# Kernel optimization log

Hardware: AMD Instinct MI355X
Metric: run time of the kernel (lower is better)

Reference implementation:

```python
import jax, jax.numpy as jnp
import numpy as np

B, TRG, SRC, ENC, TRGD = 16, 512, 1024, 1024, 1024


def setup_inputs() -> dict:
    key = jax.random.key(0)
    k1, k2, k3, k4, k5 = jax.random.split(key, 5)
    hidden = jax.random.normal(k1, (B, TRG, TRGD), dtype=jnp.float32)
    encoder_outputs = jax.random.normal(k2, (B, SRC, ENC), dtype=jnp.float32)
    encoder_value = jax.random.normal(k3, (B, SRC, TRGD), dtype=jnp.float32)
    # float {0,1} padding mask over source positions; keep first token valid
    encoder_mask = (jax.random.uniform(k4, (B, SRC)) > 0.15).astype(jnp.float32)
    encoder_mask = encoder_mask.at[:, :1].set(1.0)
    # nn.Linear(enc_dim, trg_dim, bias=False).weight -> (trg_dim, enc_dim)
    W = jax.random.normal(k5, (TRGD, ENC), dtype=jnp.float32) * (1.0 / np.sqrt(ENC))
    return {"hidden": hidden, "encoder_outputs": encoder_outputs,
            "encoder_value": encoder_value, "encoder_mask": encoder_mask, "W": W}


def reference(hidden, encoder_outputs, encoder_value, encoder_mask, W):
    # score(): method == 'general'
    proj = jnp.einsum('bse,te->bst', encoder_outputs, W)          # (B, S, trg_dim)
    proj = proj * encoder_mask[:, :, None]                        # mask-multiply projected keys
    energies = jnp.einsum('btd,bsd->bts', hidden, proj)           # (B, T, S)
    # forward(): second mask-multiply on raw energies
    attn_energies = energies * encoder_mask[:, None, :]
    # masked_softmax(x, m, -1): x*m -> stable exp -> *m -> normalize (+eps)
    x = attn_energies * encoder_mask[:, None, :]
    e = jnp.exp(x - jnp.max(x, axis=-1, keepdims=True))
    e = e * encoder_mask[:, None, :]
    attn_weights = e / (jnp.sum(e, axis=-1, keepdims=True) + 1e-6)
    context = jnp.einsum('bts,bsd->btd', attn_weights, encoder_value)  # (B, T, trg_dim)
    return context, attn_weights, attn_energies
```

## Files before the change

kernel.cpp:

```cpp
#include <hip/hip_runtime.h>
#include <math.h>

#define B_  16
#define T_  512
#define S_  1024
#define E_  1024
#define D_  1024

using short8   = __attribute__((ext_vector_type(8))) short;
using ushort4v = __attribute__((ext_vector_type(4))) unsigned short;
using float4v  = __attribute__((ext_vector_type(4))) float;

__device__ __forceinline__ unsigned short f2bf(float f) {
    unsigned u = __builtin_bit_cast(unsigned, f);
    u += 0x7fff + ((u >> 16) & 1);
    return (unsigned short)(u >> 16);
}

__device__ __forceinline__ void gl_lds16(const void* g, void* l) {
    __builtin_amdgcn_global_load_lds(
        (const __attribute__((address_space(1))) void*)g,
        (__attribute__((address_space(3))) void*)l, 16, 0, 0);
}

__global__ __launch_bounds__(256)
void cast_bf16(const float* __restrict__ src, unsigned short* __restrict__ dst, int n8)
{
    int i = blockIdx.x * 256 + threadIdx.x;
    if (i < n8) {
        float4 a = ((const float4*)src)[2 * i];
        float4 b = ((const float4*)src)[2 * i + 1];
        short8 o;
        o[0] = f2bf(a.x); o[1] = f2bf(a.y); o[2] = f2bf(a.z); o[3] = f2bf(a.w);
        o[4] = f2bf(b.x); o[5] = f2bf(b.y); o[6] = f2bf(b.z); o[7] = f2bf(b.w);
        ((short8*)dst)[i] = o;
    }
}

__global__ __launch_bounds__(256)
void transpose_cast(const float* __restrict__ src, unsigned short* __restrict__ dst,
                    int R, int C, long long sSrc, long long sDst)
{
    __shared__ unsigned short tile[64][65];
    const int z = blockIdx.z;
    src += (long long)z * sSrc;
    dst += (long long)z * sDst;
    const int c0 = blockIdx.x * 64;
    const int r0 = blockIdx.y * 64;
    const int t = threadIdx.x;

    #pragma unroll
    for (int it = 0; it < 4; ++it) {
        int r  = (t >> 4) + it * 16;
        int c4 = (t & 15) << 2;
        float4 v = *(const float4*)&src[(long long)(r0 + r) * C + c0 + c4];
        tile[r][c4 + 0] = f2bf(v.x);
        tile[r][c4 + 1] = f2bf(v.y);
        tile[r][c4 + 2] = f2bf(v.z);
        tile[r][c4 + 3] = f2bf(v.w);
    }
    __syncthreads();
    #pragma unroll
    for (int it = 0; it < 2; ++it) {
        int c  = (t >> 3) + it * 32;
        int r8 = (t & 7) << 3;
        short8 sv;
        #pragma unroll
        for (int j = 0; j < 8; ++j) sv[j] = (short)tile[r8 + j][c];
        *(short8*)&dst[(long long)(c0 + c) * R + r0 + r8] = sv;
    }
}

template<bool OUT_BF16, bool CMASK>
__global__ __launch_bounds__(256, 2)
void mfma_gemm_bf(const unsigned short* __restrict__ Ap,
                  const unsigned short* __restrict__ Bp,
                  const float* __restrict__ mask, void* __restrict__ Cp,
                  int N, int K,
                  long long sA, long long sB, long long sC, int maskStride)
{
    __shared__ unsigned short Asl[2][2 * 128 * 32];
    __shared__ unsigned short Bsl[2][2 * 128 * 32];

    const int z    = blockIdx.z;
    const int col0 = blockIdx.x * 128;
    const int row0 = blockIdx.y * 128;
    const int t    = threadIdx.x;
    const int lane = t & 63;
    const int wave = t >> 6;

    const unsigned short* A  = Ap + z * sA + (long long)row0 * K;
    const unsigned short* Bm = Bp + z * sB + (long long)col0 * K;

    const int rs  = t >> 2;
    const int kcs = (t & 3) << 3;
    const unsigned ldsW = wave * 1024;

    const int wm = (wave >> 1) * 64;
    const int wn = (wave & 1) * 64;
    const int fr = lane & 15;
    const int fg = lane >> 4;

    float4v acc[4][4];
    #pragma unroll
    for (int i = 0; i < 4; ++i)
        #pragma unroll
        for (int j = 0; j < 4; ++j)
            acc[i][j] = (float4v)0.0f;

    auto STAGE = [&](int bufi, int k0) {
        #pragma unroll
        for (int j = 0; j < 2; ++j) {
            #pragma unroll
            for (int it = 0; it < 2; ++it) {
                const int r = rs + it * 64;
                const long long goff = (long long)r * K + k0 + j * 32 + kcs;
                const unsigned loff = j * 8192 + it * 4096 + ldsW;
                gl_lds16(A  + goff, (char*)&Asl[bufi][0] + loff);
                gl_lds16(Bm + goff, (char*)&Bsl[bufi][0] + loff);
            }
        }
    };

    auto COMPUTE = [&](int bufi) {
        short8 af[2][4], bfr[2][4];
        #pragma unroll
        for (int j = 0; j < 2; ++j) {
            #pragma unroll
            for (int mi = 0; mi < 4; ++mi)
                af[j][mi] = *(const short8*)&Asl[bufi][j * 4096 + (wm + mi * 16 + fr) * 32 + fg * 8];
            #pragma unroll
            for (int ni = 0; ni < 4; ++ni)
                bfr[j][ni] = *(const short8*)&Bsl[bufi][j * 4096 + (wn + ni * 16 + fr) * 32 + fg * 8];
        }
        #pragma unroll
        for (int j = 0; j < 2; ++j)
            #pragma unroll
            for (int mi = 0; mi < 4; ++mi)
                #pragma unroll
                for (int ni = 0; ni < 4; ++ni)
                    acc[mi][ni] = __builtin_amdgcn_mfma_f32_16x16x32_bf16(af[j][mi], bfr[j][ni], acc[mi][ni], 0, 0, 0);
    };

    STAGE(0, 0);
    __syncthreads();

    int buf = 0;
    for (int k0 = 64; k0 <= K; k0 += 64) {
        if (k0 < K) STAGE(buf ^ 1, k0);
        COMPUTE(buf);
        __syncthreads();
        buf ^= 1;
    }

    float mv[4];
    #pragma unroll
    for (int ni = 0; ni < 4; ++ni) {
        int ocol = col0 + wn + ni * 16 + fr;
        mv[ni] = CMASK ? mask[(long long)z * maskStride + ocol] : 1.0f;
    }
    #pragma unroll
    for (int mi = 0; mi < 4; ++mi) {
        #pragma unroll
        for (int ni = 0; ni < 4; ++ni) {
            int ocol = col0 + wn + ni * 16 + fr;
            #pragma unroll
            for (int r = 0; r < 4; ++r) {
                int orow = row0 + wm + mi * 16 + fg * 4 + r;
                float v = acc[mi][ni][r] * mv[ni];
                if (OUT_BF16)
                    ((unsigned short*)Cp)[z * sC + (long long)orow * N + ocol] = f2bf(v);
                else
                    ((float*)Cp)[z * sC + (long long)orow * N + ocol] = v;
            }
        }
    }
}

__global__ __launch_bounds__(256)
void softmax_mask(const float* __restrict__ x, const float* __restrict__ mask,
                  float* __restrict__ w, unsigned short* __restrict__ wbf)
{
    const int row = blockIdx.x;
    const int b   = row >> 9;
    const float* xr = x    + (long long)row * S_;
    const float* mr = mask + (long long)b * S_;
    float*       wr = w    + (long long)row * S_;
    const int tid = threadIdx.x;

    float4 xv = ((const float4*)xr)[tid];
    float4 mv = ((const float4*)mr)[tid];

    float lmax = fmaxf(fmaxf(xv.x, xv.y), fmaxf(xv.z, xv.w));
    #pragma unroll
    for (int off = 32; off; off >>= 1)
        lmax = fmaxf(lmax, __shfl_xor(lmax, off, 64));

    __shared__ float red[4];
    const int wave = tid >> 6, lane = tid & 63;
    if (lane == 0) red[wave] = lmax;
    __syncthreads();
    const float rmax = fmaxf(fmaxf(red[0], red[1]), fmaxf(red[2], red[3]));

    float e0 = expf(xv.x - rmax) * mv.x;
    float e1 = expf(xv.y - rmax) * mv.y;
    float e2 = expf(xv.z - rmax) * mv.z;
    float e3 = expf(xv.w - rmax) * mv.w;

    float lsum = (e0 + e1) + (e2 + e3);
    #pragma unroll
    for (int off = 32; off; off >>= 1)
        lsum += __shfl_xor(lsum, off, 64);

    __syncthreads();
    if (lane == 0) red[wave] = lsum;
    __syncthreads();
    const float rsum = (red[0] + red[1]) + (red[2] + red[3]);
    const float inv = 1.0f / (rsum + 1e-6f);

    float4 o;
    o.x = e0 * inv; o.y = e1 * inv; o.z = e2 * inv; o.w = e3 * inv;
    ((float4*)wr)[tid] = o;
    if (wbf) {
        ushort4v u;
        u[0] = f2bf(o.x); u[1] = f2bf(o.y); u[2] = f2bf(o.z); u[3] = f2bf(o.w);
        ((ushort4v*)(wbf + (long long)row * S_))[tid] = u;
    }
}

constexpr int FBM = 64, FBN = 64, FBK = 16;
template<bool BT, bool CMASK>
__global__ __launch_bounds__(256)
void gemm_f32(const float* __restrict__ A, const float* __restrict__ Bm,
              const float* __restrict__ mask, float* __restrict__ C,
              int N_dim, int K_dim,
              long long sA, long long sB, long long sC, int maskStride)
{
    const int bz = blockIdx.z;
    A  += (long long)bz * sA;
    Bm += (long long)bz * sB;
    C  += (long long)bz * sC;
    __shared__ float As[FBK][FBM];
    __shared__ float Bs[FBK][FBN];
    const int tid  = threadIdx.x;
    const int row0 = blockIdx.y * FBM;
    const int col0 = blockIdx.x * FBN;
    const int lrow = tid >> 2;
    const int lk   = (tid & 3) << 2;
    const int bk = tid >> 4;
    const int bn = (tid & 15) << 2;
    const int tx = tid & 15;
    const int ty = tid >> 4;
    float acc[4][4] = {};
    const float* Aptr = A + (long long)(row0 + lrow) * K_dim + lk;
    const float* Bptr = BT ? (Bm + (long long)(col0 + lrow) * K_dim + lk)
                           : (Bm + (long long)bk * N_dim + col0 + bn);
    for (int k0 = 0; k0 < K_dim; k0 += FBK) {
        float4 av = *(const float4*)(Aptr + k0);
        As[lk + 0][lrow] = av.x; As[lk + 1][lrow] = av.y;
        As[lk + 2][lrow] = av.z; As[lk + 3][lrow] = av.w;
        if (BT) {
            float4 bv = *(const float4*)(Bptr + k0);
            Bs[lk + 0][lrow] = bv.x; Bs[lk + 1][lrow] = bv.y;
            Bs[lk + 2][lrow] = bv.z; Bs[lk + 3][lrow] = bv.w;
        } else {
            float4 bv = *(const float4*)(Bptr + (long long)k0 * N_dim);
            *(float4*)&Bs[bk][bn] = bv;
        }
        __syncthreads();
        #pragma unroll
        for (int k = 0; k < FBK; ++k) {
            float4 a4 = *(const float4*)&As[k][ty << 2];
            float4 b4 = *(const float4*)&Bs[k][tx << 2];
            float ar[4] = {a4.x, a4.y, a4.z, a4.w};
            float br[4] = {b4.x, b4.y, b4.z, b4.w};
            #pragma unroll
            for (int i = 0; i < 4; ++i)
                #pragma unroll
                for (int j = 0; j < 4; ++j)
                    acc[i][j] = fmaf(ar[i], br[j], acc[i][j]);
        }
        __syncthreads();
    }
    float mvv[4] = {1.f, 1.f, 1.f, 1.f};
    if (CMASK) {
        #pragma unroll
        for (int j = 0; j < 4; ++j)
            mvv[j] = mask[(long long)bz * maskStride + col0 + (tx << 2) + j];
    }
    #pragma unroll
    for (int i = 0; i < 4; ++i) {
        const int r = row0 + (ty << 2) + i;
        float4 o;
        o.x = acc[i][0] * mvv[0]; o.y = acc[i][1] * mvv[1];
        o.z = acc[i][2] * mvv[2]; o.w = acc[i][3] * mvv[3];
        *(float4*)&C[(long long)r * N_dim + col0 + (tx << 2)] = o;
    }
}

extern "C" void kernel_launch(void* const* d_in, const int* in_sizes, int n_in,
                              void* d_out, int out_size, void* d_ws, size_t ws_size,
                              hipStream_t stream)
{
    const float* hidden = (const float*)d_in[0];
    const float* eo     = (const float*)d_in[1];
    const float* ev     = (const float*)d_in[2];
    const float* mask   = (const float*)d_in[3];
    const float* W      = (const float*)d_in[4];

    float* out = (float*)d_out;
    const long long CTX = (long long)B_ * T_ * D_;
    float* ctx = out;
    float* aw  = out + CTX;
    float* ae  = out + 2 * CTX;

    dim3 blk(256);
    const size_t MB = 1024ull * 1024ull;
    const size_t NEED_FAST = 64 * MB;

    if (ws_size >= NEED_FAST) {
        char* ws = (char*)d_ws;
        unsigned short* Hbf  = (unsigned short*)(ws);
        unsigned short* WT   = (unsigned short*)(ws + 16 * MB);
        unsigned short* EObf = (unsigned short*)(ws);
        unsigned short* EVT  = (unsigned short*)(ws + 16 * MB);
        unsigned short* G    = (unsigned short*)(ws + 48 * MB);
        unsigned short* AWbf = (unsigned short*)(ws + 48 * MB);

        cast_bf16<<<dim3((B_ * T_ * D_ / 8 + 255) / 256), blk, 0, stream>>>(
            hidden, Hbf, B_ * T_ * D_ / 8);
        transpose_cast<<<dim3(E_ / 64, D_ / 64, 1), blk, 0, stream>>>(
            W, WT, D_, E_, 0, 0);

        mfma_gemm_bf<true, false><<<dim3(E_ / 128, (B_ * T_) / 128, 1), blk, 0, stream>>>(
            Hbf, WT, nullptr, G, E_, D_, 0, 0, 0, 0);

        cast_bf16<<<dim3((B_ * S_ * E_ / 8 + 255) / 256), blk, 0, stream>>>(
            eo, EObf, B_ * S_ * E_ / 8);

        mfma_gemm_bf<false, true><<<dim3(S_ / 128, T_ / 128, B_), blk, 0, stream>>>(
            G, EObf, mask, ae, S_, E_,
            (long long)T_ * E_, (long long)S_ * E_, (long long)T_ * S_, S_);

        transpose_cast<<<dim3(D_ / 64, S_ / 64, B_), blk, 0, stream>>>(
            ev, EVT, S_, D_, (long long)S_ * D_, (long long)D_ * S_);

        softmax_mask<<<dim3(B_ * T_), blk, 0, stream>>>(ae, mask, aw, AWbf);

        mfma_gemm_bf<false, false><<<dim3(D_ / 128, T_ / 128, B_), blk, 0, stream>>>(
            AWbf, EVT, nullptr, ctx, D_, S_,
            (long long)T_ * S_, (long long)D_ * S_, (long long)T_ * D_, 0);
    } else {
        float* G = aw;
        gemm_f32<false, false><<<dim3(E_ / FBN, (B_ * T_) / FBM, 1), blk, 0, stream>>>(
            hidden, W, nullptr, G, E_, D_, 0, 0, 0, 0);
        gemm_f32<true, true><<<dim3(S_ / FBN, T_ / FBM, B_), blk, 0, stream>>>(
            G, eo, mask, ae, S_, E_,
            (long long)T_ * E_, (long long)S_ * E_, (long long)T_ * S_, S_);
        softmax_mask<<<dim3(B_ * T_), blk, 0, stream>>>(ae, mask, aw, nullptr);
        gemm_f32<false, false><<<dim3(D_ / FBN, T_ / FBM, B_), blk, 0, stream>>>(
            aw, ev, nullptr, ctx, D_, S_,
            (long long)T_ * S_, (long long)S_ * D_, (long long)T_ * D_, 0);
    }
}
```

Measured before the change: 322.4 us.

## Fuse fp32-to-bf16 casts into GEMM staging and merge transpose kernels

New measurement: 338.3 us. 1.05x slower.

```diff
diff --git a/kernel.cpp b/kernel.cpp
--- a/kernel.cpp
+++ b/kernel.cpp
@@ -8,7 +8,6 @@
 #define D_  1024
 
 using short8   = __attribute__((ext_vector_type(8))) short;
-using ushort4v = __attribute__((ext_vector_type(4))) unsigned short;
 using float4v  = __attribute__((ext_vector_type(4))) float;
 
 __device__ __forceinline__ unsigned short f2bf(float f) {
@@ -24,27 +23,16 @@
 }
 
 __global__ __launch_bounds__(256)
-void cast_bf16(const float* __restrict__ src, unsigned short* __restrict__ dst, int n8)
-{
-    int i = blockIdx.x * 256 + threadIdx.x;
-    if (i < n8) {
-        float4 a = ((const float4*)src)[2 * i];
-        float4 b = ((const float4*)src)[2 * i + 1];
-        short8 o;
-        o[0] = f2bf(a.x); o[1] = f2bf(a.y); o[2] = f2bf(a.z); o[3] = f2bf(a.w);
-        o[4] = f2bf(b.x); o[5] = f2bf(b.y); o[6] = f2bf(b.z); o[7] = f2bf(b.w);
-        ((short8*)dst)[i] = o;
-    }
-}
-
-__global__ __launch_bounds__(256)
-void transpose_cast(const float* __restrict__ src, unsigned short* __restrict__ dst,
-                    int R, int C, long long sSrc, long long sDst)
+void prep_transposes(const float* __restrict__ W, unsigned short* __restrict__ WT,
+                     const float* __restrict__ ev, unsigned short* __restrict__ EVT)
 {
     __shared__ unsigned short tile[64][65];
     const int z = blockIdx.z;
-    src += (long long)z * sSrc;
-    dst += (long long)z * sDst;
+    const float* src;
+    unsigned short* dst;
+    if (z == 16) { src = W; dst = WT; }
+    else         { src = ev + (long long)z * S_ * D_; dst = EVT + (long long)z * D_ * S_; }
+    const int RC = 1024;
     const int c0 = blockIdx.x * 64;
     const int r0 = blockIdx.y * 64;
     const int t = threadIdx.x;
@@ -53,7 +41,7 @@
     for (int it = 0; it < 4; ++it) {
         int r  = (t >> 4) + it * 16;
         int c4 = (t & 15) << 2;
-        float4 v = *(const float4*)&src[(long long)(r0 + r) * C + c0 + c4];
+        float4 v = *(const float4*)&src[(long long)(r0 + r) * RC + c0 + c4];
         tile[r][c4 + 0] = f2bf(v.x);
         tile[r][c4 + 1] = f2bf(v.y);
         tile[r][c4 + 2] = f2bf(v.z);
@@ -67,17 +55,16 @@
         short8 sv;
         #pragma unroll
         for (int j = 0; j < 8; ++j) sv[j] = (short)tile[r8 + j][c];
-        *(short8*)&dst[(long long)(c0 + c) * R + r0 + r8] = sv;
-    }
-}
-
-template<bool OUT_BF16, bool CMASK>
+        *(short8*)&dst[(long long)(c0 + c) * RC + r0 + r8] = sv;
+    }
+}
+
+template<bool A_F32, bool B_F32, bool OUT_BF16, bool CMASK>
 __global__ __launch_bounds__(256, 2)
-void mfma_gemm_bf(const unsigned short* __restrict__ Ap,
-                  const unsigned short* __restrict__ Bp,
-                  const float* __restrict__ mask, void* __restrict__ Cp,
-                  int N, int K,
-                  long long sA, long long sB, long long sC, int maskStride)
+void mfma_gemm2(const void* __restrict__ Ap, const void* __restrict__ Bp,
+                const float* __restrict__ mask, void* __restrict__ Cp,
+                int N, int K,
+                long long sA, long long sB, long long sC, int maskStride)
 {
     __shared__ unsigned short Asl[2][2 * 128 * 32];
     __shared__ unsigned short Bsl[2][2 * 128 * 32];
@@ -89,8 +76,12 @@
     const int lane = t & 63;
     const int wave = t >> 6;
 
-    const unsigned short* A  = Ap + z * sA + (long long)row0 * K;
-    const unsigned short* Bm = Bp + z * sB + (long long)col0 * K;
+    const unsigned short* Ab = A_F32 ? nullptr
+        : (const unsigned short*)Ap + z * sA + (long long)row0 * K;
+    const float* Af = A_F32 ? (const float*)Ap + z * sA + (long long)row0 * K : nullptr;
+    const unsigned short* Bb = B_F32 ? nullptr
+        : (const unsigned short*)Bp + z * sB + (long long)col0 * K;
+    const float* Bf = B_F32 ? (const float*)Bp + z * sB + (long long)col0 * K : nullptr;
 
     const int rs  = t >> 2;
     const int kcs = (t & 3) << 3;
@@ -108,27 +99,64 @@
         for (int j = 0; j < 4; ++j)
             acc[i][j] = (float4v)0.0f;
 
-    auto STAGE = [&](int bufi, int k0) {
-        #pragma unroll
-        for (int j = 0; j < 2; ++j) {
+    float4 aReg[2][2][2];
+    float4 bReg[2][2][2];
+
+    auto STAGE_LOAD = [&](int bufi, int k0) {
+        #pragma unroll
+        for (int j = 0; j < 2; ++j)
+            #pragma unroll
+            for (int it = 0; it < 2; ++it) {
+                const int r = rs + it * 64;
+                const long long goff = (long long)r * K + k0 + j * 32 + kcs;
+                if constexpr (A_F32) {
+                    aReg[j][it][0] = *(const float4*)(Af + goff);
+                    aReg[j][it][1] = *(const float4*)(Af + goff + 4);
+                }
+                if constexpr (B_F32) {
+                    bReg[j][it][0] = *(const float4*)(Bf + goff);
+                    bReg[j][it][1] = *(const float4*)(Bf + goff + 4);
+                }
+            }
+        #pragma unroll
+        for (int j = 0; j < 2; ++j)
             #pragma unroll
             for (int it = 0; it < 2; ++it) {
                 const int r = rs + it * 64;
                 const long long goff = (long long)r * K + k0 + j * 32 + kcs;
                 const unsigned loff = j * 8192 + it * 4096 + ldsW;
-                gl_lds16(A  + goff, (char*)&Asl[bufi][0] + loff);
-                gl_lds16(Bm + goff, (char*)&Bsl[bufi][0] + loff);
+                if constexpr (!A_F32) gl_lds16(Ab + goff, (char*)&Asl[bufi][0] + loff);
+                if constexpr (!B_F32) gl_lds16(Bb + goff, (char*)&Bsl[bufi][0] + loff);
             }
-        }
     };
 
+    auto cvt8 = [](float4 a, float4 b) -> short8 {
+        short8 o;
+        o[0] = f2bf(a.x); o[1] = f2bf(a.y); o[2] = f2bf(a.z); o[3] = f2bf(a.w);
+        o[4] = f2bf(b.x); o[5] = f2bf(b.y); o[6] = f2bf(b.z); o[7] = f2bf(b.w);
+        return o;
+    };
+
+    auto STAGE_WRITE = [&](int bufi) {
+        #pragma unroll
+        for (int j = 0; j < 2; ++j)
+            #pragma unroll
+            for (int it = 0; it < 2; ++it) {
+                const unsigned loff = j * 8192 + it * 4096 + ldsW + lane * 16;
+                if constexpr (A_F32)
+                    *(short8*)((char*)&Asl[bufi][0] + loff) = cvt8(aReg[j][it][0], aReg[j][it][1]);
+                if constexpr (B_F32)
+                    *(short8*)((char*)&Bsl[bufi][0] + loff) = cvt8(bReg[j][it][0], bReg[j][it][1]);
+            }
+    };
+
     auto COMPUTE = [&](int bufi) {
-        short8 af[2][4], bfr[2][4];
+        short8 afr[2][4], bfr[2][4];
         #pragma unroll
         for (int j = 0; j < 2; ++j) {
             #pragma unroll
             for (int mi = 0; mi < 4; ++mi)
-                af[j][mi] = *(const short8*)&Asl[bufi][j * 4096 + (wm + mi * 16 + fr) * 32 + fg * 8];
+                afr[j][mi] = *(const short8*)&Asl[bufi][j * 4096 + (wm + mi * 16 + fr) * 32 + fg * 8];
             #pragma unroll
             for (int ni = 0; ni < 4; ++ni)
                 bfr[j][ni] = *(const short8*)&Bsl[bufi][j * 4096 + (wn + ni * 16 + fr) * 32 + fg * 8];
@@ -139,16 +167,18 @@
             for (int mi = 0; mi < 4; ++mi)
                 #pragma unroll
                 for (int ni = 0; ni < 4; ++ni)
-                    acc[mi][ni] = __builtin_amdgcn_mfma_f32_16x16x32_bf16(af[j][mi], bfr[j][ni], acc[mi][ni], 0, 0, 0);
+                    acc[mi][ni] = __builtin_amdgcn_mfma_f32_16x16x32_bf16(afr[j][mi], bfr[j][ni], acc[mi][ni], 0, 0, 0);
     };
 
-    STAGE(0, 0);
+    STAGE_LOAD(0, 0);
+    STAGE_WRITE(0);
     __syncthreads();
 
     int buf = 0;
     for (int k0 = 64; k0 <= K; k0 += 64) {
-        if (k0 < K) STAGE(buf ^ 1, k0);
+        if (k0 < K) STAGE_LOAD(buf ^ 1, k0);
         COMPUTE(buf);
+        if (k0 < K) STAGE_WRITE(buf ^ 1);
         __syncthreads();
         buf ^= 1;
     }
@@ -179,7 +209,7 @@
 
 __global__ __launch_bounds__(256)
 void softmax_mask(const float* __restrict__ x, const float* __restrict__ mask,
-                  float* __restrict__ w, unsigned short* __restrict__ wbf)
+                  float* __restrict__ w)
 {
     const int row = blockIdx.x;
     const int b   = row >> 9;
@@ -221,11 +251,6 @@
     float4 o;
     o.x = e0 * inv; o.y = e1 * inv; o.z = e2 * inv; o.w = e3 * inv;
     ((float4*)wr)[tid] = o;
-    if (wbf) {
-        ushort4v u;
-        u[0] = f2bf(o.x); u[1] = f2bf(o.y); u[2] = f2bf(o.z); u[3] = f2bf(o.w);
-        ((ushort4v*)(wbf + (long long)row * S_))[tid] = u;
-    }
 }
 
 constexpr int FBM = 64, FBN = 64, FBK = 16;
@@ -316,39 +341,30 @@
 
     dim3 blk(256);
     const size_t MB = 1024ull * 1024ull;
-    const size_t NEED_FAST = 64 * MB;
+    const size_t NEED_FAST = 50 * MB;
 
     if (ws_size >= NEED_FAST) {
         char* ws = (char*)d_ws;
-        unsigned short* Hbf  = (unsigned short*)(ws);
-        unsigned short* WT   = (unsigned short*)(ws + 16 * MB);
-        unsigned short* EObf = (unsigned short*)(ws);
-        unsigned short* EVT  = (unsigned short*)(ws + 16 * MB);
-        unsigned short* G    = (unsigned short*)(ws + 48 * MB);
-        unsigned short* AWbf = (unsigned short*)(ws + 48 * MB);
-
-        cast_bf16<<<dim3((B_ * T_ * D_ / 8 + 255) / 256), blk, 0, stream>>>(
-            hidden, Hbf, B_ * T_ * D_ / 8);
-        transpose_cast<<<dim3(E_ / 64, D_ / 64, 1), blk, 0, stream>>>(
-            W, WT, D_, E_, 0, 0);
-
-        mfma_gemm_bf<true, false><<<dim3(E_ / 128, (B_ * T_) / 128, 1), blk, 0, stream>>>(
-            Hbf, WT, nullptr, G, E_, D_, 0, 0, 0, 0);
-
-        cast_bf16<<<dim3((B_ * S_ * E_ / 8 + 255) / 256), blk, 0, stream>>>(
-            eo, EObf, B_ * S_ * E_ / 8);
-
-        mfma_gemm_bf<false, true><<<dim3(S_ / 128, T_ / 128, B_), blk, 0, stream>>>(
-            G, EObf, mask, ae, S_, E_,
+        unsigned short* WT  = (unsigned short*)(ws);
+        unsigned short* EVT = (unsigned short*)(ws + 2 * MB);
+        unsigned short* G   = (unsigned short*)(ws + 34 * MB);
+
+        prep_transposes<<<dim3(16, 16, 17), blk, 0, stream>>>(W, WT, ev, EVT);
+
+        mfma_gemm2<true, false, true, false>
+            <<<dim3(E_ / 128, (B_ * T_) / 128, 1), blk, 0, stream>>>(
+            hidden, WT, nullptr, G, E_, D_, 0, 0, 0, 0);
+
+        mfma_gemm2<false, true, false, true>
+            <<<dim3(S_ / 128, T_ / 128, B_), blk, 0, stream>>>(
+            G, eo, mask, ae, S_, E_,
             (long long)T_ * E_, (long long)S_ * E_, (long long)T_ * S_, S_);
 
-        transpose_cast<<<dim3(D_ / 64, S_ / 64, B_), blk, 0, stream>>>(
-            ev, EVT, S_, D_, (long long)S_ * D_, (long long)D_ * S_);
-
-        softmax_mask<<<dim3(B_ * T_), blk, 0, stream>>>(ae, mask, aw, AWbf);
-
-        mfma_gemm_bf<false, false><<<dim3(D_ / 128, T_ / 128, B_), blk, 0, stream>>>(
-            AWbf, EVT, nullptr, ctx, D_, S_,
+        softmax_mask<<<dim3(B_ * T_), blk, 0, stream>>>(ae, mask, aw);
+
+        mfma_gemm2<true, false, false, false>
+            <<<dim3(D_ / 128, T_ / 128, B_), blk, 0, stream>>>(
+            aw, EVT, nullptr, ctx, D_, S_,
             (long long)T_ * S_, (long long)D_ * S_, (long long)T_ * D_, 0);
     } else {
         float* G = aw;
@@ -357,7 +373,7 @@
         gemm_f32<true, true><<<dim3(S_ / FBN, T_ / FBM, B_), blk, 0, stream>>>(
             G, eo, mask, ae, S_, E_,
             (long long)T_ * E_, (long long)S_ * E_, (long long)T_ * S_, S_);
-        softmax_mask<<<dim3(B_ * T_), blk, 0, stream>>>(ae, mask, aw, nullptr);
+        softmax_mask<<<dim3(B_ * T_), blk, 0, stream>>>(ae, mask, aw);
         gemm_f32<false, false><<<dim3(D_ / FBN, T_ / FBM, B_), blk, 0, stream>>>(
             aw, ev, nullptr, ctx, D_, S_,
             (long long)T_ * S_, (long long)S_ * D_, (long long)T_ * D_, 0);
```

## Use fine-grained vmcnt waits and split barriers in bf16 GEMM main loop

Applied to the files above, without the earlier changes.

Result: no change. 325.3 us (+0.9%).

```diff
diff --git a/kernel.cpp b/kernel.cpp
--- a/kernel.cpp
+++ b/kernel.cpp
@@ -110,7 +110,7 @@
 
     auto STAGE = [&](int bufi, int k0) {
         #pragma unroll
-        for (int j = 0; j < 2; ++j) {
+        for (int j = 0; j < 2; ++j)
             #pragma unroll
             for (int it = 0; it < 2; ++it) {
                 const int r = rs + it * 64;
@@ -119,37 +119,44 @@
                 gl_lds16(A  + goff, (char*)&Asl[bufi][0] + loff);
                 gl_lds16(Bm + goff, (char*)&Bsl[bufi][0] + loff);
             }
-        }
     };
 
-    auto COMPUTE = [&](int bufi) {
-        short8 af[2][4], bfr[2][4];
+    STAGE(0, 0);
+    int buf = 0;
+    const int NT = K >> 6;
+
+    for (int ti = 0; ti < NT; ++ti) {
+        if (ti + 1 < NT) {
+            STAGE(buf ^ 1, (ti + 1) << 6);
+            asm volatile("s_waitcnt vmcnt(8)" ::: "memory");
+        } else {
+            asm volatile("s_waitcnt vmcnt(0)" ::: "memory");
+        }
+        __builtin_amdgcn_s_barrier();
+        asm volatile("" ::: "memory");
+
+        short8 af[2][4], bfv[2][4];
         #pragma unroll
         for (int j = 0; j < 2; ++j) {
             #pragma unroll
             for (int mi = 0; mi < 4; ++mi)
-                af[j][mi] = *(const short8*)&Asl[bufi][j * 4096 + (wm + mi * 16 + fr) * 32 + fg * 8];
+                af[j][mi]  = *(const short8*)&Asl[buf][j * 4096 + (wm + mi * 16 + fr) * 32 + fg * 8];
             #pragma unroll
             for (int ni = 0; ni < 4; ++ni)
-                bfr[j][ni] = *(const short8*)&Bsl[bufi][j * 4096 + (wn + ni * 16 + fr) * 32 + fg * 8];
-        }
+                bfv[j][ni] = *(const short8*)&Bsl[buf][j * 4096 + (wn + ni * 16 + fr) * 32 + fg * 8];
+        }
+        asm volatile("s_waitcnt lgkmcnt(0)" ::: "memory");
+        __builtin_amdgcn_sched_barrier(0);
+        __builtin_amdgcn_s_barrier();
+        asm volatile("" ::: "memory");
+
         #pragma unroll
         for (int j = 0; j < 2; ++j)
             #pragma unroll
             for (int mi = 0; mi < 4; ++mi)
                 #pragma unroll
                 for (int ni = 0; ni < 4; ++ni)
-                    acc[mi][ni] = __builtin_amdgcn_mfma_f32_16x16x32_bf16(af[j][mi], bfr[j][ni], acc[mi][ni], 0, 0, 0);
-    };
-
-    STAGE(0, 0);
-    __syncthreads();
-
-    int buf = 0;
-    for (int k0 = 64; k0 <= K; k0 += 64) {
-        if (k0 < K) STAGE(buf ^ 1, k0);
-        COMPUTE(buf);
-        __syncthreads();
+                    acc[mi][ni] = __builtin_amdgcn_mfma_f32_16x16x32_bf16(af[j][mi], bfv[j][ni], acc[mi][ni], 0, 0, 0);
         buf ^= 1;
     }
 
```
